# Optimization experiments

Hardware: AMD Instinct MI355X
Metric: run time of the kernel (lower is better)

Reference implementation:

```python
import jax, jax.numpy as jnp
import numpy as np

CH = 256
K = 8
INNER = CH // K  # 32


def setup_inputs() -> dict:
    key = jax.random.key(0)
    ks = jax.random.split(key, 9)
    B, C, H, W = 4, CH, 64, 64
    s = 0.02
    return {
        "x": jax.random.normal(ks[0], (B, C, H, W), dtype=jnp.float32),
        "wq": jax.random.normal(ks[1], (INNER, C), dtype=jnp.float32) * s,
        "bq": jnp.zeros((INNER,), dtype=jnp.float32),
        "wk": jax.random.normal(ks[2], (INNER, C), dtype=jnp.float32) * s,
        "bk": jnp.zeros((INNER,), dtype=jnp.float32),
        "wv": jax.random.normal(ks[3], (INNER, C), dtype=jnp.float32) * s,
        "bv": jnp.zeros((INNER,), dtype=jnp.float32),
        "wo": jax.random.normal(ks[4], (C, INNER), dtype=jnp.float32) * s,
        "bo": jnp.zeros((C,), dtype=jnp.float32),
    }


def reference(x, wq, bq, wk, bk, wv, bv, wo, bo):
    B, C, H, W = x.shape
    N = H * W
    xf = x.reshape(B, C, N)
    # 1x1 convs == channel matmuls
    q = jnp.einsum("oc,bcn->bon", wq, xf) + bq[None, :, None]  # [B, inner, N]
    k = jnp.einsum("oc,bcn->bon", wk, xf) + bk[None, :, None]
    v = jnp.einsum("oc,bcn->bon", wv, xf) + bv[None, :, None]
    # energy[b,i,j] = <q[:,i], k[:,j]> (unscaled, as in original)
    energy = jnp.einsum("bci,bcj->bij", q, k)  # [B, N, N]
    attn = jax.nn.softmax(energy, axis=-1)
    # out[b,c,i] = sum_j v[b,c,j] * attn[b,i,j]  (bmm with attn^T)
    out = jnp.einsum("bcj,bij->bci", v, attn)  # [B, inner, N]
    out = jnp.einsum("oc,bcn->bon", wo, out) + bo[None, :, None]  # [B, C, N]
    return out.reshape(B, C, H, W)
```

## Files before the change

### kernel.cpp

```cpp
#include <hip/hip_runtime.h>

#define NB 4
#define NC 256
#define NI 32
#define NN 4096
#define NSPLIT 8
#define KVQ (NN / NSPLIT)

typedef short s4v __attribute__((ext_vector_type(4)));
typedef short s8v __attribute__((ext_vector_type(8)));
typedef float f16v __attribute__((ext_vector_type(16)));
typedef unsigned u4v __attribute__((ext_vector_type(4)));

__device__ __forceinline__ unsigned short f2bf(float f) {
  unsigned u = __builtin_bit_cast(unsigned, f);
  return (unsigned short)((u + 0x7FFFu + ((u >> 16) & 1u)) >> 16);
}

__device__ __forceinline__ float fast_exp2(float x) {
  float r;
  asm("v_exp_f32 %0, %1" : "=v"(r) : "v"(x));
  return r;
}

__global__ __launch_bounds__(256) void qkv_proj(
    const float* __restrict__ x,
    const float* __restrict__ wq, const float* __restrict__ bq,
    const float* __restrict__ wk, const float* __restrict__ bk,
    const float* __restrict__ wv, const float* __restrict__ bv,
    unsigned short* __restrict__ Qb, unsigned short* __restrict__ Kb,
    unsigned short* __restrict__ Vt) {
  const int tid = threadIdx.x;
  const int ph = blockIdx.x >> 8;
  const int proj = ph >> 1;
  const int half = ph & 1;
  const int bt = blockIdx.x & 255;
  const int b = bt >> 6;
  const int n = (bt & 63) * 64 + (tid & 63);
  const int obu = __builtin_amdgcn_readfirstlane(half * 16 + (tid >> 6) * 4);

  const float* w;
  const float* bias;
  if (proj == 0) { w = wq; bias = bq; }
  else if (proj == 1) { w = wk; bias = bk; }
  else { w = wv; bias = bv; }
  const float* wp = w + (size_t)obu * NC;

  float acc[4] = {};
  const float* xp = x + ((size_t)b * NC) * NN + n;
#pragma unroll 4
  for (int c0 = 0; c0 < NC; c0 += 4) {
    const float xv0 = xp[(size_t)(c0 + 0) * NN];
    const float xv1 = xp[(size_t)(c0 + 1) * NN];
    const float xv2 = xp[(size_t)(c0 + 2) * NN];
    const float xv3 = xp[(size_t)(c0 + 3) * NN];
#pragma unroll
    for (int e = 0; e < 4; ++e) {
      const float4 w4 = *reinterpret_cast<const float4*>(&wp[e * NC + c0]);
      acc[e] += w4.x * xv0 + w4.y * xv1 + w4.z * xv2 + w4.w * xv3;
    }
  }

  if (proj < 2) {
    const float sc = proj ? 1.44269504089f : 1.0f;
    s4v pv;
#pragma unroll
    for (int e = 0; e < 4; ++e) pv[e] = (short)f2bf((acc[e] + bias[obu + e]) * sc);
    unsigned short* dst = proj == 0 ? Qb : Kb;
    *reinterpret_cast<s4v*>(&dst[((size_t)b * NN + n) * NI + obu]) = pv;
  } else {
#pragma unroll
    for (int e = 0; e < 4; ++e)
      Vt[((size_t)b * NI + obu + e) * NN + n] = f2bf(acc[e] + bias[obu + e]);
  }
}

__global__ __launch_bounds__(256) void attn_part(
    const unsigned short* __restrict__ Qb, const unsigned short* __restrict__ Kb,
    const unsigned short* __restrict__ Vt,
    unsigned short* __restrict__ Opart, float* __restrict__ Lpart) {
  const int tid = threadIdx.x;
  const int split = blockIdx.x >> 7;
  const int bt = blockIdx.x & 127;
  const int b = bt >> 5;
  const int qw = ((bt & 31) << 7) + ((tid >> 6) << 5);
  const int lane = tid & 63;
  const int l31 = lane & 31;
  const int hi = lane >> 5;

  const unsigned short* qp = Qb + ((size_t)b * NN + qw + l31) * NI + 8 * hi;
  const s8v qf0 = *reinterpret_cast<const s8v*>(qp);
  const s8v qf1 = *reinterpret_cast<const s8v*>(qp + 16);

  const unsigned short* kp = Kb + ((size_t)b * NN + (size_t)split * KVQ + l31) * NI + 8 * hi;
  const unsigned short* vp = Vt + ((size_t)b * NI + l31) * NN + (size_t)split * KVQ + 8 * hi;

  const f16v zero16 = {};
  f16v oacc = {};
  float lsum = 0.f;

#pragma unroll 4
  for (int kv = 0; kv < KVQ; kv += 32) {
    const s8v kf0 = *reinterpret_cast<const s8v*>(kp + (size_t)kv * NI);
    const s8v kf1 = *reinterpret_cast<const s8v*>(kp + (size_t)kv * NI + 16);
    const s8v vf0 = *reinterpret_cast<const s8v*>(vp + kv);
    const s8v vf1 = *reinterpret_cast<const s8v*>(vp + kv + 16);

    f16v S = __builtin_amdgcn_mfma_f32_32x32x16_bf16(kf0, qf0, zero16, 0, 0, 0);
    S = __builtin_amdgcn_mfma_f32_32x32x16_bf16(kf1, qf1, S, 0, 0, 0);

    float p[16];
#pragma unroll
    for (int r = 0; r < 16; ++r) p[r] = fast_exp2(S[r]);
    float t0 = (p[0] + p[1]) + (p[2] + p[3]);
    float t1 = (p[4] + p[5]) + (p[6] + p[7]);
    float t2 = (p[8] + p[9]) + (p[10] + p[11]);
    float t3 = (p[12] + p[13]) + (p[14] + p[15]);
    lsum += (t0 + t1) + (t2 + t3);

    unsigned d[8];
#pragma unroll
    for (int j = 0; j < 8; ++j)
      asm("v_cvt_pk_bf16_f32 %0, %1, %2" : "=v"(d[j]) : "v"(p[2 * j]), "v"(p[2 * j + 1]));
    asm("v_permlane32_swap_b32 %0, %1" : "+v"(d[0]), "+v"(d[2]));
    asm("v_permlane32_swap_b32 %0, %1" : "+v"(d[1]), "+v"(d[3]));
    asm("v_permlane32_swap_b32 %0, %1" : "+v"(d[4]), "+v"(d[6]));
    asm("v_permlane32_swap_b32 %0, %1" : "+v"(d[5]), "+v"(d[7]));

    const u4v a0 = {d[0], d[1], d[2], d[3]};
    const u4v a1 = {d[4], d[5], d[6], d[7]};
    const s8v pa0 = __builtin_bit_cast(s8v, a0);
    const s8v pa1 = __builtin_bit_cast(s8v, a1);

    oacc = __builtin_amdgcn_mfma_f32_32x32x16_bf16(pa0, vf0, oacc, 0, 0, 0);
    oacc = __builtin_amdgcn_mfma_f32_32x32x16_bf16(pa1, vf1, oacc, 0, 0, 0);
  }

  lsum += __shfl_xor(lsum, 32, 64);

  unsigned short* op = Opart + (((size_t)split * NB + b) * NN + qw) * NI + l31;
#pragma unroll
  for (int r = 0; r < 16; ++r) {
    const int qr = (r & 3) + 8 * (r >> 2) + 4 * hi;
    op[(size_t)qr * NI] = f2bf(oacc[r]);
  }
  if (hi == 0)
    Lpart[((size_t)split * NB + b) * NN + qw + l31] = lsum;
}

__global__ __launch_bounds__(256) void combine_proj(
    const unsigned short* __restrict__ Opart, const float* __restrict__ Lpart,
    const float* __restrict__ wo, const float* __restrict__ bo,
    float* __restrict__ out) {
  __shared__ __align__(16) float o_lds[NI][65];
  __shared__ float linv[64];
  const int tid = threadIdx.x;
  const int g2 = blockIdx.x >> 8;
  const int bt = blockIdx.x & 255;
  const int b = bt >> 6;
  const int q0 = (bt & 63) * 64;

  {
    const int qs = tid >> 2, cg = tid & 3;
    float s[8] = {};
#pragma unroll
    for (int sp = 0; sp < NSPLIT; ++sp) {
      const s8v v = *reinterpret_cast<const s8v*>(
          &Opart[(((size_t)sp * NB + b) * NN + q0 + qs) * NI + cg * 8]);
#pragma unroll
      for (int e = 0; e < 8; ++e) {
        const unsigned u = (unsigned)(unsigned short)v[e];
        s[e] += __builtin_bit_cast(float, u << 16);
      }
    }
#pragma unroll
    for (int e = 0; e < 8; ++e) o_lds[cg * 8 + e][qs] = s[e];
  }
  if (tid < 64) {
    float l = 0.f;
#pragma unroll
    for (int sp = 0; sp < NSPLIT; ++sp)
      l += Lpart[((size_t)sp * NB + b) * NN + q0 + tid];
    linv[tid] = 1.0f / l;
  }
  __syncthreads();

  const int q = tid & 63;
  const float il = linv[q];
  float xv[NI];
#pragma unroll
  for (int c = 0; c < NI; ++c) xv[c] = o_lds[c][q] * il;

  float* op2 = out + ((size_t)b * NC) * NN + q0 + q;
  const int co0 = g2 * 32 + (tid >> 6) * 8;
#pragma unroll
  for (int cc = 0; cc < 8; ++cc) {
    const int co = co0 + cc;
    float a = bo[co];
#pragma unroll
    for (int c4 = 0; c4 < 8; ++c4) {
      const float4 w4 = *reinterpret_cast<const float4*>(&wo[co * NI + c4 * 4]);
      a += w4.x * xv[c4 * 4] + w4.y * xv[c4 * 4 + 1] +
           w4.z * xv[c4 * 4 + 2] + w4.w * xv[c4 * 4 + 3];
    }
    op2[(size_t)co * NN] = a;
  }
}

extern "C" void kernel_launch(void* const* d_in, const int* in_sizes, int n_in,
                              void* d_out, int out_size, void* d_ws, size_t ws_size,
                              hipStream_t stream) {
  const float* x  = (const float*)d_in[0];
  const float* wq = (const float*)d_in[1];
  const float* bq = (const float*)d_in[2];
  const float* wk = (const float*)d_in[3];
  const float* bk = (const float*)d_in[4];
  const float* wv = (const float*)d_in[5];
  const float* bv = (const float*)d_in[6];
  const float* wo = (const float*)d_in[7];
  const float* bo = (const float*)d_in[8];
  float* out = (float*)d_out;

  unsigned short* Qb = (unsigned short*)d_ws;
  unsigned short* Kb = Qb + (size_t)NB * NN * NI;
  unsigned short* Vt = Kb + (size_t)NB * NN * NI;
  unsigned short* Opart = Vt + (size_t)NB * NI * NN;
  float* Lpart = (float*)(Opart + (size_t)NSPLIT * NB * NN * NI);

  qkv_proj<<<3 * 2 * NB * (NN / 64), 256, 0, stream>>>(x, wq, bq, wk, bk, wv, bv, Qb, Kb, Vt);
  attn_part<<<NSPLIT * NB * (NN / 128), 256, 0, stream>>>(Qb, Kb, Vt, Opart, Lpart);
  combine_proj<<<8 * NB * (NN / 64), 256, 0, stream>>>(Opart, Lpart, wo, bo, out);
}
```

Measured before the change: 149.5 us.

## Compute QKV projection with bf16 MFMA and store V in tiled layout

The scalar-FMA QKV projection kernel is replaced by an MFMA version. Each block handles 32 positions, the channel reduction is split across 4 waves, and the partial sums are combined through shared memory. x is read once per block for all three projections instead of six times, and x and the weights are cast to bf16 before the matmul. V is now written in a 32x32 tiled layout so attn_part loads V fragments from contiguous tiles. The bf16 rounding of x and the weights adds precision loss, and the grid is smaller (512 blocks).

```diff
diff --git a/kernel.cpp b/kernel.cpp
--- a/kernel.cpp
+++ b/kernel.cpp
@@ -23,61 +23,110 @@
   return r;
 }
 
-__global__ __launch_bounds__(256) void qkv_proj(
+__device__ __forceinline__ unsigned cvtpk(float lo, float hi) {
+  unsigned r;
+  asm("v_cvt_pk_bf16_f32 %0, %1, %2" : "=v"(r) : "v"(lo), "v"(hi));
+  return r;
+}
+
+__global__ __launch_bounds__(256) void qkv_mfma(
     const float* __restrict__ x,
     const float* __restrict__ wq, const float* __restrict__ bq,
     const float* __restrict__ wk, const float* __restrict__ bk,
     const float* __restrict__ wv, const float* __restrict__ bv,
     unsigned short* __restrict__ Qb, unsigned short* __restrict__ Kb,
-    unsigned short* __restrict__ Vt) {
+    unsigned short* __restrict__ V3) {
+  __shared__ float part[4][3][32][33];
   const int tid = threadIdx.x;
-  const int ph = blockIdx.x >> 8;
-  const int proj = ph >> 1;
-  const int half = ph & 1;
-  const int bt = blockIdx.x & 255;
-  const int b = bt >> 6;
-  const int n = (bt & 63) * 64 + (tid & 63);
-  const int obu = __builtin_amdgcn_readfirstlane(half * 16 + (tid >> 6) * 4);
-
-  const float* w;
-  const float* bias;
-  if (proj == 0) { w = wq; bias = bq; }
-  else if (proj == 1) { w = wk; bias = bk; }
-  else { w = wv; bias = bv; }
-  const float* wp = w + (size_t)obu * NC;
-
-  float acc[4] = {};
-  const float* xp = x + ((size_t)b * NC) * NN + n;
-#pragma unroll 4
-  for (int c0 = 0; c0 < NC; c0 += 4) {
-    const float xv0 = xp[(size_t)(c0 + 0) * NN];
-    const float xv1 = xp[(size_t)(c0 + 1) * NN];
-    const float xv2 = xp[(size_t)(c0 + 2) * NN];
-    const float xv3 = xp[(size_t)(c0 + 3) * NN];
-#pragma unroll
-    for (int e = 0; e < 4; ++e) {
-      const float4 w4 = *reinterpret_cast<const float4*>(&wp[e * NC + c0]);
-      acc[e] += w4.x * xv0 + w4.y * xv1 + w4.z * xv2 + w4.w * xv3;
-    }
-  }
-
-  if (proj < 2) {
-    const float sc = proj ? 1.44269504089f : 1.0f;
-    s4v pv;
-#pragma unroll
-    for (int e = 0; e < 4; ++e) pv[e] = (short)f2bf((acc[e] + bias[obu + e]) * sc);
-    unsigned short* dst = proj == 0 ? Qb : Kb;
-    *reinterpret_cast<s4v*>(&dst[((size_t)b * NN + n) * NI + obu]) = pv;
-  } else {
-#pragma unroll
-    for (int e = 0; e < 4; ++e)
-      Vt[((size_t)b * NI + obu + e) * NN + n] = f2bf(acc[e] + bias[obu + e]);
+  const int w = tid >> 6;
+  const int lane = tid & 63;
+  const int l31 = lane & 31;
+  const int hi = lane >> 5;
+  const int b = blockIdx.x >> 7;
+  const int nb = blockIdx.x & 127;
+  const int n0 = nb * 32;
+
+  const float* xb = x + (size_t)b * NC * NN + n0 + l31;
+
+  f16v accQ = {}, accK = {}, accV = {};
+#pragma unroll
+  for (int j = 0; j < 4; ++j) {
+    const int c0 = w * 64 + j * 16;
+    float xe[8];
+#pragma unroll
+    for (int e = 0; e < 8; ++e) xe[e] = xb[(size_t)(c0 + 8 * hi + e) * NN];
+    u4v xp;
+#pragma unroll
+    for (int e2 = 0; e2 < 4; ++e2) xp[e2] = cvtpk(xe[2 * e2], xe[2 * e2 + 1]);
+    const s8v xf = __builtin_bit_cast(s8v, xp);
+
+    const int wo_ = l31 * NC + c0 + 8 * hi;
+    {
+      const float4 a = *reinterpret_cast<const float4*>(&wq[wo_]);
+      const float4 c = *reinterpret_cast<const float4*>(&wq[wo_ + 4]);
+      u4v wp = {cvtpk(a.x, a.y), cvtpk(a.z, a.w), cvtpk(c.x, c.y), cvtpk(c.z, c.w)};
+      accQ = __builtin_amdgcn_mfma_f32_32x32x16_bf16(__builtin_bit_cast(s8v, wp), xf, accQ, 0, 0, 0);
+    }
+    {
+      const float4 a = *reinterpret_cast<const float4*>(&wk[wo_]);
+      const float4 c = *reinterpret_cast<const float4*>(&wk[wo_ + 4]);
+      u4v wp = {cvtpk(a.x, a.y), cvtpk(a.z, a.w), cvtpk(c.x, c.y), cvtpk(c.z, c.w)};
+      accK = __builtin_amdgcn_mfma_f32_32x32x16_bf16(__builtin_bit_cast(s8v, wp), xf, accK, 0, 0, 0);
+    }
+    {
+      const float4 a = *reinterpret_cast<const float4*>(&wv[wo_]);
+      const float4 c = *reinterpret_cast<const float4*>(&wv[wo_ + 4]);
+      u4v wp = {cvtpk(a.x, a.y), cvtpk(a.z, a.w), cvtpk(c.x, c.y), cvtpk(c.z, c.w)};
+      accV = __builtin_amdgcn_mfma_f32_32x32x16_bf16(__builtin_bit_cast(s8v, wp), xf, accV, 0, 0, 0);
+    }
+  }
+
+#pragma unroll
+  for (int r = 0; r < 16; ++r) {
+    const int row = (r & 3) + 8 * (r >> 2) + 4 * hi;
+    part[w][0][row][l31] = accQ[r];
+    part[w][1][row][l31] = accK[r];
+    part[w][2][row][l31] = accV[r];
+  }
+  __syncthreads();
+
+  {
+    const int n_l = tid >> 3;
+    const int cg = (tid & 7) * 4;
+    float sq[4] = {}, sk[4] = {};
+#pragma unroll
+    for (int ww = 0; ww < 4; ++ww)
+#pragma unroll
+      for (int jj = 0; jj < 4; ++jj) {
+        sq[jj] += part[ww][0][cg + jj][n_l];
+        sk[jj] += part[ww][1][cg + jj][n_l];
+      }
+    s4v qv, kv;
+#pragma unroll
+    for (int jj = 0; jj < 4; ++jj) {
+      qv[jj] = (short)f2bf(sq[jj] + bq[cg + jj]);
+      kv[jj] = (short)f2bf((sk[jj] + bk[cg + jj]) * 1.44269504089f);
+    }
+    *reinterpret_cast<s4v*>(&Qb[((size_t)b * NN + n0 + n_l) * NI + cg]) = qv;
+    *reinterpret_cast<s4v*>(&Kb[((size_t)b * NN + n0 + n_l) * NI + cg]) = kv;
+  }
+  {
+    const int n_l = tid & 31;
+    const int cb = (tid >> 5) * 4;
+    unsigned short* vdst = V3 + (((size_t)b * 128 + nb) * 32) * 32;
+#pragma unroll
+    for (int i = 0; i < 4; ++i) {
+      const int c = cb + i;
+      float s = part[0][2][c][n_l] + part[1][2][c][n_l] +
+                part[2][2][c][n_l] + part[3][2][c][n_l];
+      vdst[(size_t)c * 32 + n_l] = f2bf(s + bv[c]);
+    }
   }
 }
 
 __global__ __launch_bounds__(256) void attn_part(
     const unsigned short* __restrict__ Qb, const unsigned short* __restrict__ Kb,
-    const unsigned short* __restrict__ Vt,
+    const unsigned short* __restrict__ V3,
     unsigned short* __restrict__ Opart, float* __restrict__ Lpart) {
   const int tid = threadIdx.x;
   const int split = blockIdx.x >> 7;
@@ -93,7 +142,8 @@
   const s8v qf1 = *reinterpret_cast<const s8v*>(qp + 16);
 
   const unsigned short* kp = Kb + ((size_t)b * NN + (size_t)split * KVQ + l31) * NI + 8 * hi;
-  const unsigned short* vp = Vt + ((size_t)b * NI + l31) * NN + (size_t)split * KVQ + 8 * hi;
+  const unsigned short* vp =
+      V3 + (((size_t)b * 128 + (split * KVQ) / 32) * 32 + l31) * 32 + 8 * hi;
 
   const f16v zero16 = {};
   f16v oacc = {};
@@ -103,8 +153,8 @@
   for (int kv = 0; kv < KVQ; kv += 32) {
     const s8v kf0 = *reinterpret_cast<const s8v*>(kp + (size_t)kv * NI);
     const s8v kf1 = *reinterpret_cast<const s8v*>(kp + (size_t)kv * NI + 16);
-    const s8v vf0 = *reinterpret_cast<const s8v*>(vp + kv);
-    const s8v vf1 = *reinterpret_cast<const s8v*>(vp + kv + 16);
+    const s8v vf0 = *reinterpret_cast<const s8v*>(vp + (size_t)kv * 32);
+    const s8v vf1 = *reinterpret_cast<const s8v*>(vp + (size_t)kv * 32 + 16);
 
     f16v S = __builtin_amdgcn_mfma_f32_32x32x16_bf16(kf0, qf0, zero16, 0, 0, 0);
     S = __builtin_amdgcn_mfma_f32_32x32x16_bf16(kf1, qf1, S, 0, 0, 0);
@@ -120,8 +170,7 @@
 
     unsigned d[8];
 #pragma unroll
-    for (int j = 0; j < 8; ++j)
-      asm("v_cvt_pk_bf16_f32 %0, %1, %2" : "=v"(d[j]) : "v"(p[2 * j]), "v"(p[2 * j + 1]));
+    for (int j = 0; j < 8; ++j) d[j] = cvtpk(p[2 * j], p[2 * j + 1]);
     asm("v_permlane32_swap_b32 %0, %1" : "+v"(d[0]), "+v"(d[2]));
     asm("v_permlane32_swap_b32 %0, %1" : "+v"(d[1]), "+v"(d[3]));
     asm("v_permlane32_swap_b32 %0, %1" : "+v"(d[4]), "+v"(d[6]));
@@ -129,11 +178,8 @@
 
     const u4v a0 = {d[0], d[1], d[2], d[3]};
     const u4v a1 = {d[4], d[5], d[6], d[7]};
-    const s8v pa0 = __builtin_bit_cast(s8v, a0);
-    const s8v pa1 = __builtin_bit_cast(s8v, a1);
-
-    oacc = __builtin_amdgcn_mfma_f32_32x32x16_bf16(pa0, vf0, oacc, 0, 0, 0);
-    oacc = __builtin_amdgcn_mfma_f32_32x32x16_bf16(pa1, vf1, oacc, 0, 0, 0);
+    oacc = __builtin_amdgcn_mfma_f32_32x32x16_bf16(__builtin_bit_cast(s8v, a0), vf0, oacc, 0, 0, 0);
+    oacc = __builtin_amdgcn_mfma_f32_32x32x16_bf16(__builtin_bit_cast(s8v, a1), vf1, oacc, 0, 0, 0);
   }
 
   lsum += __shfl_xor(lsum, 32, 64);
@@ -223,11 +269,11 @@
 
   unsigned short* Qb = (unsigned short*)d_ws;
   unsigned short* Kb = Qb + (size_t)NB * NN * NI;
-  unsigned short* Vt = Kb + (size_t)NB * NN * NI;
-  unsigned short* Opart = Vt + (size_t)NB * NI * NN;
+  unsigned short* V3 = Kb + (size_t)NB * NN * NI;
+  unsigned short* Opart = V3 + (size_t)NB * NN * NI;
   float* Lpart = (float*)(Opart + (size_t)NSPLIT * NB * NN * NI);
 
-  qkv_proj<<<3 * 2 * NB * (NN / 64), 256, 0, stream>>>(x, wq, bq, wk, bk, wv, bv, Qb, Kb, Vt);
-  attn_part<<<NSPLIT * NB * (NN / 128), 256, 0, stream>>>(Qb, Kb, Vt, Opart, Lpart);
+  qkv_mfma<<<NB * (NN / 32), 256, 0, stream>>>(x, wq, bq, wk, bk, wv, bv, Qb, Kb, V3);
+  attn_part<<<NSPLIT * NB * (NN / 128), 256, 0, stream>>>(Qb, Kb, V3, Opart, Lpart);
   combine_proj<<<8 * NB * (NN / 64), 256, 0, stream>>>(Opart, Lpart, wo, bo, out);
 }
```

Result: faster. 129.3 us (-13.5%).
